# Optimization experiments

Hardware: AMD Instinct MI355X
Metric: run time of the kernel (lower is better)

## Reference

```python
import jax, jax.numpy as jnp
import numpy as np

# init config (from init_kwargs)
EMBED_DIM = 32          # D
N_PIXELS = 8192         # N
KERNEL_BANDWIDTH = 0.5
STEP_SIZE = 0.5
NB_ITERATIONS = 5


def setup_inputs() -> dict:
    key = jax.random.key(0)
    # embeddings live in a bounded ball (margin-based loss) -> scale down so
    # exp(bw * <x_i, x_j>) stays numerically tame, like trained embeddings.
    x_in = jax.random.normal(key, (EMBED_DIM, N_PIXELS), dtype=jnp.float32) * 0.1
    return {"x_in": x_in}


def reference(x_in):
    """Mean-shift iterations on D x N embeddings.

    Each step: K = exp(bw * x^T x)  (N x N, symmetric)
               x <- step * x @ (K / colsum(K)) + (1 - step) * x
    which is exactly x @ (step * K @ inv(diag(K^T 1)) + (1-step) * I)
    from the original torch code, without materializing diag/inverse/eye.
    """
    step = jnp.float32(STEP_SIZE)
    bw = jnp.float32(KERNEL_BANDWIDTH)

    def body(x, _):
        kernel = jnp.exp(bw * (x.T @ x))          # [N, N]
        deg = kernel.sum(axis=0)                  # column sums d_j, [N]
        x_new = step * (x @ kernel) / deg + (1.0 - step) * x  # [D, N]
        return x_new, None

    x_out, _ = jax.lax.scan(body, x_in, None, length=NB_ITERATIONS)
    return x_out
```

## Files before the change

kernel.cpp:

```cpp
#include <hip/hip_runtime.h>
#include <hip/hip_bf16.h>
#include <math.h>


typedef short bf16x8 __attribute__((ext_vector_type(8)));
typedef float f32x16 __attribute__((ext_vector_type(16)));
typedef int v2i __attribute__((ext_vector_type(2)));

#define NPIX 8192
#define DIM 32
#define NITER 5
#define SCH 16
#define CHUNK (NPIX / SCH)
#define HALF 128
#define HALVES (CHUNK / HALF)
#define WAVES 4
#define ALPHA 0.8493219f

#if __has_builtin(__builtin_amdgcn_exp2f)
#define EXP2(x) __builtin_amdgcn_exp2f(x)
#else
#define EXP2(x) exp2f(x)
#endif

__device__ __forceinline__ void glds16(const uint4* g, uint4* l) {
#if __has_builtin(__builtin_amdgcn_global_load_lds)
    __builtin_amdgcn_global_load_lds((const __attribute__((address_space(1))) void*)g,
                                     (__attribute__((address_space(3))) void*)l,
                                     16, 0, 0);
#else
    *l = *g;
#endif
}

__device__ inline unsigned cvtpk(float lo, float hi) {
    unsigned r;
    asm("v_cvt_pk_bf16_f32 %0, %1, %2" : "=v"(r) : "v"(lo), "v"(hi));
    return r;
}

__device__ inline void swap32(unsigned a, unsigned b, unsigned& x, unsigned& y) {
#if __has_builtin(__builtin_amdgcn_permlane32_swap)
    v2i r = __builtin_amdgcn_permlane32_swap((int)a, (int)b, false, false);
    x = (unsigned)r.x;
    y = (unsigned)r.y;
#else
    unsigned bs = __shfl_xor(b, 32);
    unsigned as = __shfl_xor(a, 32);
    int hi = (int)(threadIdx.x & 63) >> 5;
    x = hi ? bs : a;
    y = hi ? b : as;
#endif
}

__device__ inline unsigned short f2bf(float f) {
    unsigned u = __float_as_uint(f);
    unsigned r = (u + 0x7FFFu + ((u >> 16) & 1u)) >> 16;
    return (unsigned short)r;
}

__device__ inline unsigned pk2(float a, float b) {
    return (unsigned)f2bf(a) | ((unsigned)f2bf(b) << 16);
}

union U4 { uint4 q; bf16x8 v; };

__global__ __launch_bounds__(256, 4) void k_ms(const unsigned short* __restrict__ kq,
                                               const unsigned short* __restrict__ vv,
                                               float* __restrict__ party,
                                               float* __restrict__ partd) {
    __shared__ uint4 sm[2048];
    const int tid = threadIdx.x;
    const int lane = tid & 63;
    const int lo = lane & 31, hi = lane >> 5;
    const int wv = tid >> 6;
    const int wbase = tid & ~63;
    const int jblk = blockIdx.x * WAVES + wv;
    const int chunk = blockIdx.y;

    const uint4* kq4 = (const uint4*)kq;
    const uint4* vv4 = (const uint4*)vv;

    U4 q0, q1;
    q0.q = kq4[jblk * 128 + lane];
    q1.q = kq4[jblk * 128 + 64 + lane];

    U4 ones;
    ones.q = make_uint4(0x3F803F80u, 0x3F803F80u, 0x3F803F80u, 0x3F803F80u);

    f32x16 z16;
#pragma unroll
    for (int r = 0; r < 16; ++r) z16[r] = 0.f;
    f32x16 y = z16;
    f32x16 dg16 = z16;

    const uint4* gk = kq4 + (size_t)chunk * CHUNK * 4;
    const uint4* gv = vv4 + (size_t)chunk * CHUNK * 4;

    auto STAGE = [&](int h, int b) {
        const uint4* gkh = gk + h * (HALF * 4);
        const uint4* gvh = gv + h * (HALF * 4);
        uint4* dK = sm + b * 1024 + wbase;
        uint4* dV = dK + 512;
#pragma unroll
        for (int r = 0; r < 2; ++r) {
            glds16(gkh + r * 256 + tid, dK + r * 256);
            glds16(gvh + r * 256 + tid, dV + r * 256);
        }
    };

    STAGE(0, 0);

    for (int h = 0; h < HALVES; ++h) {
        __builtin_amdgcn_s_barrier();
        if (h + 1 < HALVES) {
            STAGE(h + 1, (h + 1) & 1);
            asm volatile("s_waitcnt vmcnt(4)" ::: "memory");
        } else {
            asm volatile("s_waitcnt vmcnt(0)" ::: "memory");
        }
        __builtin_amdgcn_s_barrier();

        const uint4* bK = sm + ((h & 1) << 10);
        const uint4* bV = bK + 512;
#pragma unroll
        for (int t0 = 0; t0 < HALF / 32; ++t0) {
            const int t = (t0 + wv) & (HALF / 32 - 1);
            U4 ka0, ka1, vb0, vb1;
            ka0.q = bK[t * 128 + lane];
            ka1.q = bK[t * 128 + 64 + lane];
            vb0.q = bV[t * 128 + lane];
            vb1.q = bV[t * 128 + 64 + lane];

            f32x16 s;
            s = __builtin_amdgcn_mfma_f32_32x32x16_bf16(ka0.v, q0.v, z16, 0, 0, 0);
            s = __builtin_amdgcn_mfma_f32_32x32x16_bf16(ka1.v, q1.v, s, 0, 0, 0);
            float p[16];
#pragma unroll
            for (int r = 0; r < 16; ++r) p[r] = EXP2(s[r]);

#pragma unroll
            for (int ks = 0; ks < 2; ++ks) {
                const float* pb = p + ks * 8;
                unsigned a0 = cvtpk(pb[0], pb[1]);
                unsigned a1 = cvtpk(pb[2], pb[3]);
                unsigned b0 = cvtpk(pb[4], pb[5]);
                unsigned b1 = cvtpk(pb[6], pb[7]);
                unsigned w01, w45, w23, w67;
                swap32(a0, b0, w01, w45);
                swap32(a1, b1, w23, w67);
                U4 pa;
                pa.q = make_uint4(w01, w23, w45, w67);
                y = __builtin_amdgcn_mfma_f32_32x32x16_bf16(
                        pa.v, (ks ? vb1.v : vb0.v), y, 0, 0, 0);
                dg16 = __builtin_amdgcn_mfma_f32_32x32x16_bf16(
                        pa.v, ones.v, dg16, 0, 0, 0);
            }
        }
    }

    float* yrow = party + ((size_t)chunk * NPIX + (size_t)jblk * 32) * 32;
    float* drow = partd + (size_t)chunk * NPIX + (size_t)jblk * 32;
#pragma unroll
    for (int r = 0; r < 16; ++r) {
        int jr = (r & 3) + 8 * (r >> 2) + 4 * hi;
        yrow[(size_t)jr * 32 + lo] = y[r];
        if (lo == 0) drow[jr] = dg16[r];
    }
}

__global__ __launch_bounds__(256) void k_prep(const float* __restrict__ xin,
                                              float* __restrict__ xm,
                                              unsigned short* __restrict__ kq,
                                              unsigned short* __restrict__ vv) {
    const int j = blockIdx.x * 256 + threadIdx.x;
    float xv[DIM];
#pragma unroll
    for (int d = 0; d < DIM; ++d) xv[d] = xin[(size_t)d * NPIX + j];

    float4* xmr = (float4*)(xm + (size_t)j * DIM);
#pragma unroll
    for (int q = 0; q < 8; ++q)
        xmr[q] = make_float4(xv[4*q], xv[4*q+1], xv[4*q+2], xv[4*q+3]);

    uint4* kq4 = (uint4*)kq;
#pragma unroll
    for (int ks = 0; ks < 2; ++ks)
#pragma unroll
        for (int h = 0; h < 2; ++h) {
            const int b = ks * 16 + h * 8;
            kq4[(j >> 5) * 128 + ks * 64 + h * 32 + (j & 31)] =
                make_uint4(pk2(xv[b+0]*ALPHA, xv[b+1]*ALPHA), pk2(xv[b+2]*ALPHA, xv[b+3]*ALPHA),
                           pk2(xv[b+4]*ALPHA, xv[b+5]*ALPHA), pk2(xv[b+6]*ALPHA, xv[b+7]*ALPHA));
        }

    const int vbase = (j >> 5) * 1024 + ((j >> 4) & 1) * 512 + ((j >> 3) & 1) * 256 + (j & 7);
#pragma unroll
    for (int d = 0; d < DIM; ++d) vv[vbase + d * 8] = f2bf(xv[d]);
}

__global__ __launch_bounds__(256) void k_upd(const float* __restrict__ party,
                                             const float* __restrict__ partd,
                                             const float* __restrict__ xm,
                                             float* __restrict__ xm_next,
                                             unsigned short* __restrict__ kq,
                                             unsigned short* __restrict__ vv,
                                             float* __restrict__ out,
                                             int last) {
    const int t = blockIdx.x * 256 + threadIdx.x;
    const int j = t >> 2, q = t & 3;

    float4 ya = make_float4(0.f, 0.f, 0.f, 0.f);
    float4 yb = make_float4(0.f, 0.f, 0.f, 0.f);
    float dg = 0.f;
    for (int c = 0; c < SCH; ++c) {
        const float4* p4 = (const float4*)(party + ((size_t)c * NPIX + j) * 32 + q * 8);
        float4 a = p4[0], b = p4[1];
        ya.x += a.x; ya.y += a.y; ya.z += a.z; ya.w += a.w;
        yb.x += b.x; yb.y += b.y; yb.z += b.z; yb.w += b.w;
        dg += partd[(size_t)c * NPIX + j];
    }
    const float inv = 0.5f / dg;

    const float4* xr = (const float4*)(xm + (size_t)j * DIM + q * 8);
    float4 v0 = xr[0], v1 = xr[1];
    float xn[8];
    xn[0] = fmaf(ya.x, inv, 0.5f * v0.x);
    xn[1] = fmaf(ya.y, inv, 0.5f * v0.y);
    xn[2] = fmaf(ya.z, inv, 0.5f * v0.z);
    xn[3] = fmaf(ya.w, inv, 0.5f * v0.w);
    xn[4] = fmaf(yb.x, inv, 0.5f * v1.x);
    xn[5] = fmaf(yb.y, inv, 0.5f * v1.y);
    xn[6] = fmaf(yb.z, inv, 0.5f * v1.z);
    xn[7] = fmaf(yb.w, inv, 0.5f * v1.w);

    if (last) {
#pragma unroll
        for (int e = 0; e < 8; ++e) out[(size_t)(q * 8 + e) * NPIX + j] = xn[e];
        return;
    }

    float4* xw = (float4*)(xm_next + (size_t)j * DIM + q * 8);
    xw[0] = make_float4(xn[0], xn[1], xn[2], xn[3]);
    xw[1] = make_float4(xn[4], xn[5], xn[6], xn[7]);

    ((uint4*)kq)[(j >> 5) * 128 + (q >> 1) * 64 + (q & 1) * 32 + (j & 31)] =
        make_uint4(pk2(xn[0]*ALPHA, xn[1]*ALPHA), pk2(xn[2]*ALPHA, xn[3]*ALPHA),
                   pk2(xn[4]*ALPHA, xn[5]*ALPHA), pk2(xn[6]*ALPHA, xn[7]*ALPHA));

    const int vbase = (j >> 5) * 1024 + ((j >> 4) & 1) * 512 + ((j >> 3) & 1) * 256 + (j & 7);
#pragma unroll
    for (int e = 0; e < 8; ++e) vv[vbase + (q * 8 + e) * 8] = f2bf(xn[e]);
}

extern "C" void kernel_launch(void* const* d_in, const int* in_sizes, int n_in,
                              void* d_out, int out_size, void* d_ws, size_t ws_size,
                              hipStream_t stream) {
    const float* x_in = (const float*)d_in[0];
    float* out = (float*)d_out;

    const size_t nd = (size_t)NPIX * DIM;
    float* xmA = (float*)d_ws;
    float* xmB = xmA + nd;
    float* party = xmB + nd;
    float* partd = party + (size_t)SCH * NPIX * 32;
    unsigned short* kq = (unsigned short*)(partd + (size_t)SCH * NPIX);
    unsigned short* vv = kq + nd;

    k_prep<<<NPIX / 256, 256, 0, stream>>>(x_in, xmA, kq, vv);

    for (int it = 0; it < NITER; ++it) {
        const int last = (it == NITER - 1);
        k_ms<<<dim3(NPIX / (32 * WAVES), SCH), 256, 0, stream>>>(kq, vv, party, partd);
        k_upd<<<(NPIX * 4) / 256, 256, 0, stream>>>(party, partd, xmA, xmB, kq, vv, out, last);
        float* t = xmA; xmA = xmB; xmB = t;
    }
}
```

Baseline: 129.6 us.

## Widen mean-shift blocks to eight waves and store partial sums as bf16

The main kernel now runs 512-thread blocks with eight waves sharing each staged K/V tile. Each thread issues one async global-to-LDS load per tensor per stage instead of two, which halves staging traffic per output column. The partial y sums written per chunk are rounded to bf16 and decoded in the update kernel, halving that intermediate write and read traffic. The per-wave rotation of LDS tile order is removed. The bf16 partials lose precision before the cross-chunk reduction, and the larger blocks may lower occupancy.

Result: faster. 109.6 us (-15.5%).

```diff
diff --git a/kernel.cpp b/kernel.cpp
--- a/kernel.cpp
+++ b/kernel.cpp
@@ -14,7 +14,7 @@
 #define CHUNK (NPIX / SCH)
 #define HALF 128
 #define HALVES (CHUNK / HALF)
-#define WAVES 4
+#define WAVES 8
 #define ALPHA 0.8493219f
 
 #if __has_builtin(__builtin_amdgcn_exp2f)
@@ -63,11 +63,14 @@
     return (unsigned)f2bf(a) | ((unsigned)f2bf(b) << 16);
 }
 
+__device__ inline float bfl(unsigned u) { return __uint_as_float(u << 16); }
+__device__ inline float bfh(unsigned u) { return __uint_as_float(u & 0xFFFF0000u); }
+
 union U4 { uint4 q; bf16x8 v; };
 
-__global__ __launch_bounds__(256, 4) void k_ms(const unsigned short* __restrict__ kq,
+__global__ __launch_bounds__(512, 4) void k_ms(const unsigned short* __restrict__ kq,
                                                const unsigned short* __restrict__ vv,
-                                               float* __restrict__ party,
+                                               unsigned short* __restrict__ party,
                                                float* __restrict__ partd) {
     __shared__ uint4 sm[2048];
     const int tid = threadIdx.x;
@@ -101,12 +104,8 @@
         const uint4* gkh = gk + h * (HALF * 4);
         const uint4* gvh = gv + h * (HALF * 4);
         uint4* dK = sm + b * 1024 + wbase;
-        uint4* dV = dK + 512;
-#pragma unroll
-        for (int r = 0; r < 2; ++r) {
-            glds16(gkh + r * 256 + tid, dK + r * 256);
-            glds16(gvh + r * 256 + tid, dV + r * 256);
-        }
+        glds16(gkh + tid, dK);
+        glds16(gvh + tid, dK + 512);
     };
 
     STAGE(0, 0);
@@ -115,7 +114,7 @@
         __builtin_amdgcn_s_barrier();
         if (h + 1 < HALVES) {
             STAGE(h + 1, (h + 1) & 1);
-            asm volatile("s_waitcnt vmcnt(4)" ::: "memory");
+            asm volatile("s_waitcnt vmcnt(2)" ::: "memory");
         } else {
             asm volatile("s_waitcnt vmcnt(0)" ::: "memory");
         }
@@ -124,8 +123,7 @@
         const uint4* bK = sm + ((h & 1) << 10);
         const uint4* bV = bK + 512;
 #pragma unroll
-        for (int t0 = 0; t0 < HALF / 32; ++t0) {
-            const int t = (t0 + wv) & (HALF / 32 - 1);
+        for (int t = 0; t < HALF / 32; ++t) {
             U4 ka0, ka1, vb0, vb1;
             ka0.q = bK[t * 128 + lane];
             ka1.q = bK[t * 128 + 64 + lane];
@@ -159,12 +157,12 @@
         }
     }
 
-    float* yrow = party + ((size_t)chunk * NPIX + (size_t)jblk * 32) * 32;
+    unsigned short* yrow = party + ((size_t)chunk * NPIX + (size_t)jblk * 32) * 32;
     float* drow = partd + (size_t)chunk * NPIX + (size_t)jblk * 32;
 #pragma unroll
     for (int r = 0; r < 16; ++r) {
         int jr = (r & 3) + 8 * (r >> 2) + 4 * hi;
-        yrow[(size_t)jr * 32 + lo] = y[r];
+        yrow[(size_t)jr * 32 + lo] = f2bf(y[r]);
         if (lo == 0) drow[jr] = dg16[r];
     }
 }
@@ -199,7 +197,7 @@
     for (int d = 0; d < DIM; ++d) vv[vbase + d * 8] = f2bf(xv[d]);
 }
 
-__global__ __launch_bounds__(256) void k_upd(const float* __restrict__ party,
+__global__ __launch_bounds__(256) void k_upd(const unsigned short* __restrict__ party,
                                              const float* __restrict__ partd,
                                              const float* __restrict__ xm,
                                              float* __restrict__ xm_next,
@@ -210,14 +208,16 @@
     const int t = blockIdx.x * 256 + threadIdx.x;
     const int j = t >> 2, q = t & 3;
 
-    float4 ya = make_float4(0.f, 0.f, 0.f, 0.f);
-    float4 yb = make_float4(0.f, 0.f, 0.f, 0.f);
+    float ys[8];
+#pragma unroll
+    for (int e = 0; e < 8; ++e) ys[e] = 0.f;
     float dg = 0.f;
     for (int c = 0; c < SCH; ++c) {
-        const float4* p4 = (const float4*)(party + ((size_t)c * NPIX + j) * 32 + q * 8);
-        float4 a = p4[0], b = p4[1];
-        ya.x += a.x; ya.y += a.y; ya.z += a.z; ya.w += a.w;
-        yb.x += b.x; yb.y += b.y; yb.z += b.z; yb.w += b.w;
+        uint4 u = *(const uint4*)(party + ((size_t)c * NPIX + j) * 32 + q * 8);
+        ys[0] += bfl(u.x); ys[1] += bfh(u.x);
+        ys[2] += bfl(u.y); ys[3] += bfh(u.y);
+        ys[4] += bfl(u.z); ys[5] += bfh(u.z);
+        ys[6] += bfl(u.w); ys[7] += bfh(u.w);
         dg += partd[(size_t)c * NPIX + j];
     }
     const float inv = 0.5f / dg;
@@ -225,14 +225,14 @@
     const float4* xr = (const float4*)(xm + (size_t)j * DIM + q * 8);
     float4 v0 = xr[0], v1 = xr[1];
     float xn[8];
-    xn[0] = fmaf(ya.x, inv, 0.5f * v0.x);
-    xn[1] = fmaf(ya.y, inv, 0.5f * v0.y);
-    xn[2] = fmaf(ya.z, inv, 0.5f * v0.z);
-    xn[3] = fmaf(ya.w, inv, 0.5f * v0.w);
-    xn[4] = fmaf(yb.x, inv, 0.5f * v1.x);
-    xn[5] = fmaf(yb.y, inv, 0.5f * v1.y);
-    xn[6] = fmaf(yb.z, inv, 0.5f * v1.z);
-    xn[7] = fmaf(yb.w, inv, 0.5f * v1.w);
+    xn[0] = fmaf(ys[0], inv, 0.5f * v0.x);
+    xn[1] = fmaf(ys[1], inv, 0.5f * v0.y);
+    xn[2] = fmaf(ys[2], inv, 0.5f * v0.z);
+    xn[3] = fmaf(ys[3], inv, 0.5f * v0.w);
+    xn[4] = fmaf(ys[4], inv, 0.5f * v1.x);
+    xn[5] = fmaf(ys[5], inv, 0.5f * v1.y);
+    xn[6] = fmaf(ys[6], inv, 0.5f * v1.z);
+    xn[7] = fmaf(ys[7], inv, 0.5f * v1.w);
 
     if (last) {
 #pragma unroll
@@ -262,8 +262,8 @@
     const size_t nd = (size_t)NPIX * DIM;
     float* xmA = (float*)d_ws;
     float* xmB = xmA + nd;
-    float* party = xmB + nd;
-    float* partd = party + (size_t)SCH * NPIX * 32;
+    unsigned short* party = (unsigned short*)(xmB + nd);
+    float* partd = (float*)(party + (size_t)SCH * NPIX * 32);
     unsigned short* kq = (unsigned short*)(partd + (size_t)SCH * NPIX);
     unsigned short* vv = kq + nd;
 
@@ -271,7 +271,7 @@
 
     for (int it = 0; it < NITER; ++it) {
         const int last = (it == NITER - 1);
-        k_ms<<<dim3(NPIX / (32 * WAVES), SCH), 256, 0, stream>>>(kq, vv, party, partd);
+        k_ms<<<dim3(NPIX / (32 * WAVES), SCH), 512, 0, stream>>>(kq, vv, party, partd);
         k_upd<<<(NPIX * 4) / 256, 256, 0, stream>>>(party, partd, xmA, xmB, kq, vv, out, last);
         float* t = xmA; xmA = xmB; xmB = t;
     }
```
